# Kernel optimization log

Measured on AMD Instinct MI355X. Metric: run time of the kernel, lower is better.

Reference implementation:

```python
import jax, jax.numpy as jnp
import numpy as np

H = 512  # hidden_size


def setup_inputs() -> dict:
    key = jax.random.key(0)
    k1, k2, k3, k4, k5 = jax.random.split(key, 5)
    B, S = 32, 2048
    hidden = jax.random.normal(k1, (1, B, H), dtype=jnp.float32)
    encoder_outputs = jax.random.normal(k2, (B, S, 2 * H), dtype=jnp.float32)
    # nn.Linear(3H, H): weight [H, 3H], store transposed [3H, H] for x @ W
    scale_a = 1.0 / np.sqrt(3 * H)
    Wa = jax.random.uniform(k3, (3 * H, H), jnp.float32, -scale_a, scale_a)
    ba = jax.random.uniform(k4, (H,), jnp.float32, -scale_a, scale_a)
    # nn.Linear(H, 1, bias=False): weight [1, H] -> store as [H]
    scale_v = 1.0 / np.sqrt(H)
    v = jax.random.uniform(k5, (H,), jnp.float32, -scale_v, scale_v)
    return {"hidden": hidden, "encoder_outputs": encoder_outputs,
            "Wa": Wa, "ba": ba, "v": v}


def reference(hidden, encoder_outputs, Wa, ba, v):
    # hidden: [1, B, H] -> [B, H]; encoder_outputs: [B, S, 2H]
    h = jnp.squeeze(hidden, axis=0)                      # [B, H]
    # Split concat-linear into two projections (same math as cat + matmul):
    Wh, We = Wa[:H], Wa[H:]                              # [H, H], [2H, H]
    # energy: [B, S, H] = tanh(h Wh + enc We + b), h broadcast over S
    energy = jnp.tanh(h @ Wh + jnp.einsum('bse,eh->bsh', encoder_outputs, We)[..., :, :] + ba) if False else \
             jnp.tanh((h @ Wh)[:, None, :] + jnp.einsum('bse,eh->bsh', encoder_outputs, We) + ba)
    scores = jnp.einsum('bsh,h->bs', energy, v)          # [B, S]
    attention_weights = jax.nn.softmax(scores, axis=1)   # [B, S]
    context = jnp.einsum('bs,bse->be', attention_weights, encoder_outputs)  # [B, 2H]
    return context, attention_weights
```

## Files before the change

### kernel.cpp

```cpp
#include <hip/hip_runtime.h>

typedef unsigned short ushort_t;
typedef __attribute__((ext_vector_type(8))) short bf16x8;
typedef __attribute__((ext_vector_type(4))) float f32x4;

#define H 512
#define E 1024
#define S 2048
#define B 32

__device__ __forceinline__ ushort_t f2bf(float f) {
    unsigned u = __float_as_uint(f);
    unsigned r = (u + 0x7FFFu + ((u >> 16) & 1u)) >> 16;
    return (ushort_t)r;
}

__device__ __forceinline__ unsigned pkbf(float x, float y) {
    unsigned u0 = __float_as_uint(x) + 0x8000u;
    unsigned u1 = __float_as_uint(y) + 0x8000u;
    return __builtin_amdgcn_perm(u1, u0, 0x07060302u);
}

__global__ void prep_hb(const float* __restrict__ hidden, const float* __restrict__ Wa,
                        const float* __restrict__ ba, float* __restrict__ hb) {
    int b = blockIdx.x, kc = blockIdx.y, tid = threadIdx.x;
    const float* hp = hidden + b * H + kc * 64;
    float a0 = 0.f, a1 = 0.f;
    #pragma unroll 8
    for (int k = 0; k < 64; ++k) {
        float hv = hp[k];
        a0 += hv * Wa[(size_t)(kc * 64 + k) * H + tid];
        a1 += hv * Wa[(size_t)(kc * 64 + k) * H + tid + 256];
    }
    if (kc == 0) { a0 += ba[tid]; a1 += ba[tid + 256]; }
    atomicAdd(&hb[b * H + tid], a0);
    atomicAdd(&hb[b * H + tid + 256], a1);
}

__global__ void prep_wef(const float* __restrict__ Wa, ushort_t* __restrict__ wef) {
    int g = blockIdx.x * 256 + threadIdx.x;
    int kt = g >> 11, nt = (g >> 6) & 31, l = g & 63;
    int kbase = kt * 32 + ((l >> 4) << 3);
    int n = nt * 16 + (l & 15);
    #pragma unroll
    for (int j = 0; j < 8; ++j)
        wef[(size_t)g * 8 + j] = f2bf(Wa[(size_t)(H + kbase + j) * H + n]);
}

__launch_bounds__(256, 2)
__global__ void score_kernel(const float* __restrict__ enc, const ushort_t* __restrict__ wef,
                             const float* __restrict__ hb, const float* __restrict__ v,
                             float* __restrict__ scores) {
    int b = blockIdx.y;
    int s0 = blockIdx.x * 64;
    int tid = threadIdx.x;
    int wave = tid >> 6, lane = tid & 63;
    int q = lane >> 4, nl = lane & 15;

    __shared__ char arena[81920];
    float* sred = (float*)arena;

    f32x4 acc[4][8] = {};

    const char* bsrc = (const char*)wef + wave * 8192 + lane * 16;
    int r0 = wave * 16 + (lane >> 3);
    int c4 = ((lane & 7) ^ (lane >> 3)) * 4;
    const float* asrc0 = enc + ((size_t)b * S + s0 + r0) * E + c4;
    const float* asrc1 = asrc0 + 8 * E;

#define STAGE(KT, D)                                                                     \
    {                                                                                    \
        const char* bp = bsrc + (size_t)(KT) * 32768;                                    \
        char* bl = arena + (D) * 32768 + wave * 8192;                                    \
        _Pragma("unroll")                                                                \
        for (int j = 0; j < 8; ++j)                                                      \
            __builtin_amdgcn_global_load_lds(                                            \
                (const __attribute__((address_space(1))) unsigned*)(bp + j * 1024),      \
                (__attribute__((address_space(3))) unsigned*)(bl + j * 1024), 16, 0, 0); \
        char* al = arena + 65536 + (D) * 8192 + wave * 2048;                             \
        __builtin_amdgcn_global_load_lds(                                                \
            (const __attribute__((address_space(1))) unsigned*)(asrc0 + (KT) * 32),      \
            (__attribute__((address_space(3))) unsigned*)(al), 16, 0, 0);                \
        __builtin_amdgcn_global_load_lds(                                                \
            (const __attribute__((address_space(1))) unsigned*)(asrc1 + (KT) * 32),      \
            (__attribute__((address_space(3))) unsigned*)(al + 1024), 16, 0, 0);         \
    }

#define COMPUTE(CUR)                                                                     \
    {                                                                                    \
        const ushort_t* Bc = (const ushort_t*)(arena + (CUR) * 32768);                   \
        const float*    Ac = (const float*)(arena + 65536 + (CUR) * 8192);               \
        bf16x8 afr[4];                                                                   \
        _Pragma("unroll")                                                                \
        for (int mt = 0; mt < 4; ++mt) {                                                 \
            int r = mt * 16 + nl;                                                        \
            int sa = r * 8 + ((2 * q) ^ (nl & 7));                                       \
            int sb = r * 8 + ((2 * q + 1) ^ (nl & 7));                                   \
            float4 f0 = *(const float4*)(Ac + sa * 4);                                   \
            float4 f1 = *(const float4*)(Ac + sb * 4);                                   \
            uint4 u;                                                                     \
            u.x = pkbf(f0.x, f0.y); u.y = pkbf(f0.z, f0.w);                              \
            u.z = pkbf(f1.x, f1.y); u.w = pkbf(f1.z, f1.w);                              \
            afr[mt] = *(bf16x8*)&u;                                                      \
        }                                                                                \
        _Pragma("unroll")                                                                \
        for (int ntl = 0; ntl < 8; ++ntl) {                                              \
            bf16x8 bfr = *(const bf16x8*)&Bc[((wave * 8 + ntl) * 64 + lane) * 8];        \
            _Pragma("unroll")                                                            \
            for (int mt = 0; mt < 4; ++mt)                                               \
                acc[mt][ntl] = __builtin_amdgcn_mfma_f32_16x16x32_bf16(                  \
                    afr[mt], bfr, acc[mt][ntl], 0, 0, 0);                                \
        }                                                                                \
    }

    STAGE(0, 0);
    __syncthreads();
    for (int kt = 0; kt < 31; ++kt) {
        STAGE(kt + 1, (kt + 1) & 1);
        COMPUTE(kt & 1);
        __syncthreads();
    }
    COMPUTE(1);
    __syncthreads();

    float p[16];
    #pragma unroll
    for (int i = 0; i < 16; ++i) p[i] = 0.f;
    #pragma unroll
    for (int ntl = 0; ntl < 8; ++ntl) {
        int n = wave * 128 + ntl * 16 + nl;
        float hv = hb[b * H + n];
        float vv = v[n];
        #pragma unroll
        for (int mt = 0; mt < 4; ++mt)
            #pragma unroll
            for (int r = 0; r < 4; ++r)
                p[mt * 4 + r] += vv * tanhf(acc[mt][ntl][r] + hv);
    }
    #pragma unroll
    for (int off = 1; off < 16; off <<= 1) {
        #pragma unroll
        for (int i = 0; i < 16; ++i) p[i] += __shfl_xor(p[i], off, 64);
    }
    if (nl == 0) {
        #pragma unroll
        for (int mt = 0; mt < 4; ++mt)
            #pragma unroll
            for (int r = 0; r < 4; ++r)
                sred[wave * 64 + mt * 16 + q * 4 + r] = p[mt * 4 + r];
    }
    __syncthreads();
    if (tid < 64) {
        float s = sred[tid] + sred[64 + tid] + sred[128 + tid] + sred[192 + tid];
        scores[(size_t)b * S + s0 + tid] = s;
    }
#undef STAGE
#undef COMPUTE
}

__global__ void softmax_kernel(const float* __restrict__ scores, float* __restrict__ out) {
    int b = blockIdx.x, tid = threadIdx.x;
    const float* row = scores + (size_t)b * S;
    float loc[8];
    float mx = -3.4e38f;
    #pragma unroll
    for (int i = 0; i < 8; ++i) { loc[i] = row[tid + i * 256]; mx = fmaxf(mx, loc[i]); }
    #pragma unroll
    for (int off = 32; off > 0; off >>= 1) mx = fmaxf(mx, __shfl_xor(mx, off, 64));
    __shared__ float wm[4], wsm[4];
    if ((tid & 63) == 0) wm[tid >> 6] = mx;
    __syncthreads();
    mx = fmaxf(fmaxf(wm[0], wm[1]), fmaxf(wm[2], wm[3]));
    float sum = 0.f;
    #pragma unroll
    for (int i = 0; i < 8; ++i) { loc[i] = __expf(loc[i] - mx); sum += loc[i]; }
    #pragma unroll
    for (int off = 32; off > 0; off >>= 1) sum += __shfl_xor(sum, off, 64);
    if ((tid & 63) == 0) wsm[tid >> 6] = sum;
    __syncthreads();
    sum = wsm[0] + wsm[1] + wsm[2] + wsm[3];
    float inv = 1.f / sum;
    #pragma unroll
    for (int i = 0; i < 8; ++i) out[B * E + (size_t)b * S + tid + i * 256] = loc[i] * inv;
    #pragma unroll
    for (int i = 0; i < 4; ++i) out[(size_t)b * E + tid + i * 256] = 0.f;
}

__global__ void context_kernel(const float* __restrict__ enc, const float* __restrict__ w_attn,
                               float* __restrict__ out_ctx) {
    int sc = blockIdx.x, b = blockIdx.y;
    int e = threadIdx.x * 4;
    const float* w  = w_attn + (size_t)b * S + sc * 64;
    const float* ep = enc + ((size_t)b * S + sc * 64) * E + e;
    float a0 = 0.f, a1 = 0.f, a2 = 0.f, a3 = 0.f;
    #pragma unroll 8
    for (int s = 0; s < 64; ++s) {
        float ws = w[s];
        float4 x = *(const float4*)(ep + (size_t)s * E);
        a0 += ws * x.x; a1 += ws * x.y; a2 += ws * x.z; a3 += ws * x.w;
    }
    float* dst = &out_ctx[(size_t)b * E + e];
    atomicAdd(dst + 0, a0);
    atomicAdd(dst + 1, a1);
    atomicAdd(dst + 2, a2);
    atomicAdd(dst + 3, a3);
}

extern "C" void kernel_launch(void* const* d_in, const int* in_sizes, int n_in,
                              void* d_out, int out_size, void* d_ws, size_t ws_size,
                              hipStream_t stream) {
    const float* hidden = (const float*)d_in[0];
    const float* enc    = (const float*)d_in[1];
    const float* Wa     = (const float*)d_in[2];
    const float* ba     = (const float*)d_in[3];
    const float* v      = (const float*)d_in[4];
    float* out = (float*)d_out;

    char* ws = (char*)d_ws;
    ushort_t* wef = (ushort_t*)ws;
    float* hb     = (float*)(ws + (1 << 20));
    float* scores = (float*)(ws + (1 << 20) + (1 << 16));

    hipMemsetAsync(hb, 0, B * H * sizeof(float), stream);
    prep_hb<<<dim3(B, 8), 256, 0, stream>>>(hidden, Wa, ba, hb);
    prep_wef<<<256, 256, 0, stream>>>(Wa, wef);
    score_kernel<<<dim3(S / 64, B), 256, 0, stream>>>(enc, wef, hb, v, scores);
    softmax_kernel<<<B, 256, 0, stream>>>(scores, out);
    context_kernel<<<dim3(32, B), 256, 0, stream>>>(enc, out + B * E, out);
}
```

Before: 499.5 us.

## Fuse softmax and context into score kernel with split-softmax partials and register-held B

Each score block now computes a local max and sum of exponentials for its 64-row chunk and immediately multiplies the still-cached encoder rows by those weights, writing per-chunk partial contexts. A small combine kernel rescales the partials flash-style and writes the normalized attention weights. This removes the separate softmax and context kernels, their atomics, and the second full read of encoder_outputs. The B operand (bf16 weights) is now loaded straight into registers instead of staged through LDS, which shrinks shared memory and adds a deeper A pipeline. tanhf is also replaced by an exp-based fast tanh, which costs some accuracy and more register pressure.

```diff
diff --git a/kernel.cpp b/kernel.cpp
--- a/kernel.cpp
+++ b/kernel.cpp
@@ -8,6 +8,7 @@
 #define E 1024
 #define S 2048
 #define B 32
+#define NCHUNK (S / 64)
 
 __device__ __forceinline__ ushort_t f2bf(float f) {
     unsigned u = __float_as_uint(f);
@@ -19,6 +20,11 @@
     unsigned u0 = __float_as_uint(x) + 0x8000u;
     unsigned u1 = __float_as_uint(y) + 0x8000u;
     return __builtin_amdgcn_perm(u1, u0, 0x07060302u);
+}
+
+__device__ __forceinline__ float fast_tanh(float x) {
+    float e = __expf(2.f * x);
+    return 1.f - 2.f / (e + 1.f);
 }
 
 __global__ void prep_hb(const float* __restrict__ hidden, const float* __restrict__ Wa,
@@ -50,34 +56,31 @@
 __launch_bounds__(256, 2)
 __global__ void score_kernel(const float* __restrict__ enc, const ushort_t* __restrict__ wef,
                              const float* __restrict__ hb, const float* __restrict__ v,
-                             float* __restrict__ scores) {
+                             float* __restrict__ scores, float* __restrict__ mpart,
+                             float* __restrict__ lpart, float* __restrict__ ctxp) {
+    int sc = blockIdx.x;
     int b = blockIdx.y;
-    int s0 = blockIdx.x * 64;
+    int s0 = sc * 64;
     int tid = threadIdx.x;
     int wave = tid >> 6, lane = tid & 63;
     int q = lane >> 4, nl = lane & 15;
 
-    __shared__ char arena[81920];
+    __shared__ char arena[32768];
     float* sred = (float*)arena;
+    float* lds_p = (float*)arena + 256;
 
     f32x4 acc[4][8] = {};
-
-    const char* bsrc = (const char*)wef + wave * 8192 + lane * 16;
+    bf16x8 bregA[8], bregB[8];
+
     int r0 = wave * 16 + (lane >> 3);
     int c4 = ((lane & 7) ^ (lane >> 3)) * 4;
     const float* asrc0 = enc + ((size_t)b * S + s0 + r0) * E + c4;
     const float* asrc1 = asrc0 + 8 * E;
-
-#define STAGE(KT, D)                                                                     \
+    const bf16x8* bsrc = (const bf16x8*)wef + (size_t)(wave * 8) * 64 + lane;
+
+#define STAGE_A(KT)                                                                      \
     {                                                                                    \
-        const char* bp = bsrc + (size_t)(KT) * 32768;                                    \
-        char* bl = arena + (D) * 32768 + wave * 8192;                                    \
-        _Pragma("unroll")                                                                \
-        for (int j = 0; j < 8; ++j)                                                      \
-            __builtin_amdgcn_global_load_lds(                                            \
-                (const __attribute__((address_space(1))) unsigned*)(bp + j * 1024),      \
-                (__attribute__((address_space(3))) unsigned*)(bl + j * 1024), 16, 0, 0); \
-        char* al = arena + 65536 + (D) * 8192 + wave * 2048;                             \
+        char* al = arena + ((KT) & 3) * 8192 + wave * 2048;                              \
         __builtin_amdgcn_global_load_lds(                                                \
             (const __attribute__((address_space(1))) unsigned*)(asrc0 + (KT) * 32),      \
             (__attribute__((address_space(3))) unsigned*)(al), 16, 0, 0);                \
@@ -86,10 +89,13 @@
             (__attribute__((address_space(3))) unsigned*)(al + 1024), 16, 0, 0);         \
     }
 
-#define COMPUTE(CUR)                                                                     \
+#define LOADB(BREG, KT)                                                                  \
+    _Pragma("unroll")                                                                    \
+    for (int ntl = 0; ntl < 8; ++ntl) BREG[ntl] = bsrc[(size_t)(KT) * 2048 + ntl * 64];
+
+#define COMPUTE(KT, BREG)                                                                \
     {                                                                                    \
-        const ushort_t* Bc = (const ushort_t*)(arena + (CUR) * 32768);                   \
-        const float*    Ac = (const float*)(arena + 65536 + (CUR) * 8192);               \
+        const float* Ac = (const float*)(arena + ((KT) & 3) * 8192);                     \
         bf16x8 afr[4];                                                                   \
         _Pragma("unroll")                                                                \
         for (int mt = 0; mt < 4; ++mt) {                                                 \
@@ -105,22 +111,43 @@
         }                                                                                \
         _Pragma("unroll")                                                                \
         for (int ntl = 0; ntl < 8; ++ntl) {                                              \
-            bf16x8 bfr = *(const bf16x8*)&Bc[((wave * 8 + ntl) * 64 + lane) * 8];        \
             _Pragma("unroll")                                                            \
             for (int mt = 0; mt < 4; ++mt)                                               \
                 acc[mt][ntl] = __builtin_amdgcn_mfma_f32_16x16x32_bf16(                  \
-                    afr[mt], bfr, acc[mt][ntl], 0, 0, 0);                                \
+                    afr[mt], BREG[ntl], acc[mt][ntl], 0, 0, 0);                          \
         }                                                                                \
     }
 
-    STAGE(0, 0);
-    __syncthreads();
-    for (int kt = 0; kt < 31; ++kt) {
-        STAGE(kt + 1, (kt + 1) & 1);
-        COMPUTE(kt & 1);
-        __syncthreads();
-    }
-    COMPUTE(1);
+    STAGE_A(0);
+    STAGE_A(1);
+    __builtin_amdgcn_sched_barrier(0);
+    LOADB(bregA, 0);
+    __builtin_amdgcn_sched_barrier(0);
+    asm volatile("s_waitcnt vmcnt(10)" ::: "memory");
+    __builtin_amdgcn_s_barrier();
+    __builtin_amdgcn_sched_barrier(0);
+
+#define FULL_ITER(T, BCUR, BNEXT)                                                        \
+    STAGE_A((T) + 2);                                                                    \
+    __builtin_amdgcn_sched_barrier(0);                                                   \
+    LOADB(BNEXT, (T) + 1);                                                               \
+    COMPUTE((T), BCUR);                                                                  \
+    __builtin_amdgcn_sched_barrier(0);                                                   \
+    asm volatile("s_waitcnt vmcnt(10)" ::: "memory");                                    \
+    __builtin_amdgcn_s_barrier();                                                        \
+    __builtin_amdgcn_sched_barrier(0);
+
+    for (int it = 0; it < 15; ++it) {
+        FULL_ITER(it * 2, bregA, bregB);
+        FULL_ITER(it * 2 + 1, bregB, bregA);
+    }
+    LOADB(bregB, 31);
+    COMPUTE(30, bregA);
+    __builtin_amdgcn_sched_barrier(0);
+    asm volatile("s_waitcnt vmcnt(8)" ::: "memory");
+    __builtin_amdgcn_s_barrier();
+    __builtin_amdgcn_sched_barrier(0);
+    COMPUTE(31, bregB);
     __syncthreads();
 
     float p[16];
@@ -135,7 +162,7 @@
         for (int mt = 0; mt < 4; ++mt)
             #pragma unroll
             for (int r = 0; r < 4; ++r)
-                p[mt * 4 + r] += vv * tanhf(acc[mt][ntl][r] + hv);
+                p[mt * 4 + r] += vv * fast_tanh(acc[mt][ntl][r] + hv);
     }
     #pragma unroll
     for (int off = 1; off < 16; off <<= 1) {
@@ -150,60 +177,76 @@
                 sred[wave * 64 + mt * 16 + q * 4 + r] = p[mt * 4 + r];
     }
     __syncthreads();
+
     if (tid < 64) {
         float s = sred[tid] + sred[64 + tid] + sred[128 + tid] + sred[192 + tid];
         scores[(size_t)b * S + s0 + tid] = s;
-    }
-#undef STAGE
-#undef COMPUTE
-}
-
-__global__ void softmax_kernel(const float* __restrict__ scores, float* __restrict__ out) {
-    int b = blockIdx.x, tid = threadIdx.x;
-    const float* row = scores + (size_t)b * S;
-    float loc[8];
-    float mx = -3.4e38f;
-    #pragma unroll
-    for (int i = 0; i < 8; ++i) { loc[i] = row[tid + i * 256]; mx = fmaxf(mx, loc[i]); }
-    #pragma unroll
-    for (int off = 32; off > 0; off >>= 1) mx = fmaxf(mx, __shfl_xor(mx, off, 64));
-    __shared__ float wm[4], wsm[4];
-    if ((tid & 63) == 0) wm[tid >> 6] = mx;
-    __syncthreads();
-    mx = fmaxf(fmaxf(wm[0], wm[1]), fmaxf(wm[2], wm[3]));
-    float sum = 0.f;
-    #pragma unroll
-    for (int i = 0; i < 8; ++i) { loc[i] = __expf(loc[i] - mx); sum += loc[i]; }
-    #pragma unroll
-    for (int off = 32; off > 0; off >>= 1) sum += __shfl_xor(sum, off, 64);
-    if ((tid & 63) == 0) wsm[tid >> 6] = sum;
-    __syncthreads();
-    sum = wsm[0] + wsm[1] + wsm[2] + wsm[3];
-    float inv = 1.f / sum;
-    #pragma unroll
-    for (int i = 0; i < 8; ++i) out[B * E + (size_t)b * S + tid + i * 256] = loc[i] * inv;
-    #pragma unroll
-    for (int i = 0; i < 4; ++i) out[(size_t)b * E + tid + i * 256] = 0.f;
-}
-
-__global__ void context_kernel(const float* __restrict__ enc, const float* __restrict__ w_attn,
-                               float* __restrict__ out_ctx) {
-    int sc = blockIdx.x, b = blockIdx.y;
-    int e = threadIdx.x * 4;
-    const float* w  = w_attn + (size_t)b * S + sc * 64;
-    const float* ep = enc + ((size_t)b * S + sc * 64) * E + e;
-    float a0 = 0.f, a1 = 0.f, a2 = 0.f, a3 = 0.f;
+        float m = s;
+        #pragma unroll
+        for (int off = 32; off; off >>= 1) m = fmaxf(m, __shfl_xor(m, off, 64));
+        float pe = __expf(s - m);
+        lds_p[tid] = pe;
+        float l = pe;
+        #pragma unroll
+        for (int off = 32; off; off >>= 1) l += __shfl_xor(l, off, 64);
+        if (tid == 0) { mpart[b * NCHUNK + sc] = m; lpart[b * NCHUNK + sc] = l; }
+    }
+    __syncthreads();
+
+    const float* ep = enc + ((size_t)b * S + s0) * E + tid * 4;
+    float cx = 0.f, cy = 0.f, cz = 0.f, cw = 0.f;
     #pragma unroll 8
     for (int s = 0; s < 64; ++s) {
-        float ws = w[s];
+        float ps = lds_p[s];
         float4 x = *(const float4*)(ep + (size_t)s * E);
-        a0 += ws * x.x; a1 += ws * x.y; a2 += ws * x.z; a3 += ws * x.w;
-    }
-    float* dst = &out_ctx[(size_t)b * E + e];
-    atomicAdd(dst + 0, a0);
-    atomicAdd(dst + 1, a1);
-    atomicAdd(dst + 2, a2);
-    atomicAdd(dst + 3, a3);
+        cx += ps * x.x; cy += ps * x.y; cz += ps * x.z; cw += ps * x.w;
+    }
+    float4 co = {cx, cy, cz, cw};
+    *(float4*)(ctxp + ((size_t)(b * NCHUNK + sc)) * E + tid * 4) = co;
+#undef STAGE_A
+#undef LOADB
+#undef COMPUTE
+#undef FULL_ITER
+}
+
+__global__ void combine_kernel(const float* __restrict__ scores, const float* __restrict__ mpart,
+                               const float* __restrict__ lpart, const float* __restrict__ ctxp,
+                               float* __restrict__ out) {
+    int b = blockIdx.x, tid = threadIdx.x;
+    __shared__ float sscale[NCHUNK];
+    __shared__ float sml[2];
+    if (tid < NCHUNK) {
+        float m = mpart[b * NCHUNK + tid];
+        float M = m;
+        #pragma unroll
+        for (int off = 16; off; off >>= 1) M = fmaxf(M, __shfl_xor(M, off, 64));
+        float e = __expf(m - M);
+        float l = lpart[b * NCHUNK + tid] * e;
+        float L = l;
+        #pragma unroll
+        for (int off = 16; off; off >>= 1) L += __shfl_xor(L, off, 64);
+        sscale[tid] = e;
+        if (tid == 0) { sml[0] = M; sml[1] = L; }
+    }
+    __syncthreads();
+    float M = sml[0], invL = 1.0f / sml[1];
+    int e0 = tid * 4;
+    float cx = 0.f, cy = 0.f, cz = 0.f, cw = 0.f;
+    #pragma unroll 4
+    for (int i = 0; i < NCHUNK; ++i) {
+        float scv = sscale[i];
+        float4 x = *(const float4*)(ctxp + ((size_t)(b * NCHUNK + i)) * E + e0);
+        cx += scv * x.x; cy += scv * x.y; cz += scv * x.z; cw += scv * x.w;
+    }
+    float4 co = {cx * invL, cy * invL, cz * invL, cw * invL};
+    *(float4*)(out + (size_t)b * E + e0) = co;
+    const float* srow = scores + (size_t)b * S;
+    float* wrow = out + B * E + (size_t)b * S;
+    #pragma unroll
+    for (int j = 0; j < 8; ++j) {
+        int s = tid + j * 256;
+        wrow[s] = __expf(srow[s] - M) * invL;
+    }
 }
 
 extern "C" void kernel_launch(void* const* d_in, const int* in_sizes, int n_in,
@@ -220,11 +263,14 @@
     ushort_t* wef = (ushort_t*)ws;
     float* hb     = (float*)(ws + (1 << 20));
     float* scores = (float*)(ws + (1 << 20) + (1 << 16));
+    float* mpart  = (float*)(ws + (1 << 20) + (1 << 16) + (1 << 18));
+    float* lpart  = mpart + B * NCHUNK;
+    float* ctxp   = (float*)(ws + (1 << 20) + (1 << 16) + (1 << 18) + (1 << 14));
 
     hipMemsetAsync(hb, 0, B * H * sizeof(float), stream);
     prep_hb<<<dim3(B, 8), 256, 0, stream>>>(hidden, Wa, ba, hb);
     prep_wef<<<256, 256, 0, stream>>>(Wa, wef);
-    score_kernel<<<dim3(S / 64, B), 256, 0, stream>>>(enc, wef, hb, v, scores);
-    softmax_kernel<<<B, 256, 0, stream>>>(scores, out);
-    context_kernel<<<dim3(32, B), 256, 0, stream>>>(enc, out + B * E, out);
-}
+    score_kernel<<<dim3(NCHUNK, B), 256, 0, stream>>>(enc, wef, hb, v,
+                                                      scores, mpart, lpart, ctxp);
+    combine_kernel<<<B, 256, 0, stream>>>(scores, mpart, lpart, ctxp, out);
+}
```

After: 455.5 us. -8.8%, faster.
